# Performance work log

Measured on AMD Instinct MI355X. Metric: run time of the kernel, lower is better.

The kernel has to match this reference:

```python
import jax, jax.numpy as jnp
import numpy as np

B, N, F_IN, F_OUT = 8, 2048, 256, 128
ALPHA = 0.2
NEG_BIG = -9000000000000000.0


def setup_inputs() -> dict:
    key = jax.random.key(0)
    k1, k2, k3, k4 = jax.random.split(key, 4)
    X = jax.random.normal(k1, (B, N, F_IN), dtype=jnp.float32)
    # sparse-ish binary adjacency with self loops (faithful: module only needs 0/1 mask)
    A = (jax.random.uniform(k2, (B, N, N)) < 0.05).astype(jnp.float32)
    eye = jnp.eye(N, dtype=jnp.float32)[None]
    A = jnp.maximum(A, eye)
    # xavier_uniform-style init
    limW = float(np.sqrt(6.0 / (F_IN + F_OUT)))
    W = jax.random.uniform(k3, (F_IN, F_OUT), minval=-limW, maxval=limW, dtype=jnp.float32)
    lima = float(np.sqrt(6.0 / (2 * F_OUT + 1)))
    a = jax.random.uniform(k4, (2 * F_OUT, 1), minval=-lima, maxval=lima, dtype=jnp.float32)
    return {"X": X, "A": A, "W": W, "a": a}


def reference(X, A, W, a):
    # Wh: [B, N, F_OUT]
    Wh = jnp.einsum('bni,io->bno', X, W)
    # split a into source/dest halves: e_ij = leaky_relu(a1.Wh_i + a2.Wh_j)
    # (algebraically identical to cat([Wh_i, Wh_j]) @ a, avoids BxNxNx2F tensor)
    a1 = a[:F_OUT, 0]   # [F_OUT]
    a2 = a[F_OUT:, 0]   # [F_OUT]
    s1 = Wh @ a1        # [B, N]
    s2 = Wh @ a2        # [B, N]
    e = jax.nn.leaky_relu(s1[:, :, None] + s2[:, None, :], negative_slope=ALPHA)  # [B,N,N]
    e = e + NEG_BIG * (1.0 - A)
    attention = jax.nn.softmax(e, axis=-1)
    h_prime = jnp.einsum('bmn,bno->bmo', attention, Wh)
    return h_prime
```

## Files before the change

kernel.cpp:

```cpp
#include <hip/hip_runtime.h>
#include <math.h>

#define B_DIM 8
#define N_DIM 2048
#define F_IN 256
#define F_OUT 128
#define ALPHA 0.2f
#define CAP 256
#define KPAD 136

typedef __attribute__((ext_vector_type(8))) short short8;
typedef __attribute__((ext_vector_type(4))) float floatx4;

static __device__ __forceinline__ unsigned short f2bf(float f) {
    unsigned u = __float_as_uint(f);
    u += 0x7fff + ((u >> 16) & 1);
    return (unsigned short)(u >> 16);
}
static __device__ __forceinline__ float bflo(unsigned w) { return __uint_as_float(w << 16); }
static __device__ __forceinline__ float bfhi(unsigned w) { return __uint_as_float(w & 0xffff0000u); }

__global__ __launch_bounds__(256) void gemm_xw(const float* __restrict__ X,
                                               const float* __restrict__ W,
                                               const float* __restrict__ avec,
                                               unsigned short* __restrict__ Whb,
                                               float* __restrict__ s1,
                                               float* __restrict__ s2) {
    __shared__ unsigned short Wt[F_OUT][KPAD];
    const int t = threadIdx.x;
    const int lane = t & 63, wave = t >> 6;
    const int m = lane & 15, q = lane >> 4;
    const int row0 = blockIdx.x * 64 + wave * 16;

    floatx4 acc[8];
#pragma unroll
    for (int nt = 0; nt < 8; nt++) acc[nt] = (floatx4){0.f, 0.f, 0.f, 0.f};

    const int n0 = (t & 31) * 4;
    const int kb = t >> 5;

    for (int half = 0; half < 2; half++) {
        const float* Wp = W + (size_t)(half * 128 + kb) * F_OUT + n0;
#pragma unroll
        for (int i = 0; i < 16; i++) {
            float4 w = *(const float4*)(Wp + (size_t)i * 8 * F_OUT);
            int kk = kb + i * 8;
            Wt[n0 + 0][kk] = f2bf(w.x);
            Wt[n0 + 1][kk] = f2bf(w.y);
            Wt[n0 + 2][kk] = f2bf(w.z);
            Wt[n0 + 3][kk] = f2bf(w.w);
        }
        __syncthreads();

        const float* xrow = X + (size_t)(row0 + m) * F_IN + half * 128 + q * 8;
        float4 xr[8];
#pragma unroll
        for (int kt = 0; kt < 4; kt++) {
            xr[2 * kt] = *(const float4*)(xrow + kt * 32);
            xr[2 * kt + 1] = *(const float4*)(xrow + kt * 32 + 4);
        }
#pragma unroll
        for (int kt = 0; kt < 4; kt++) {
            union { unsigned short u[8]; short8 v; } af;
            float tmp[8] = {xr[2 * kt].x, xr[2 * kt].y, xr[2 * kt].z, xr[2 * kt].w,
                            xr[2 * kt + 1].x, xr[2 * kt + 1].y, xr[2 * kt + 1].z, xr[2 * kt + 1].w};
#pragma unroll
            for (int j = 0; j < 8; j++) af.u[j] = f2bf(tmp[j]);
#pragma unroll
            for (int nt = 0; nt < 8; nt++) {
                short8 bv = *(const short8*)&Wt[nt * 16 + m][kt * 32 + q * 8];
                acc[nt] = __builtin_amdgcn_mfma_f32_16x16x32_bf16(af.v, bv, acc[nt], 0, 0, 0);
            }
        }
        __syncthreads();
    }

#pragma unroll
    for (int nt = 0; nt < 8; nt++) {
#pragma unroll
        for (int r = 0; r < 4; r++) {
            int row = row0 + q * 4 + r;
            Whb[(size_t)row * F_OUT + nt * 16 + m] = f2bf(acc[nt][r]);
        }
    }
    float a1v[8], a2v[8];
#pragma unroll
    for (int nt = 0; nt < 8; nt++) {
        a1v[nt] = avec[nt * 16 + m];
        a2v[nt] = avec[F_OUT + nt * 16 + m];
    }
#pragma unroll
    for (int r = 0; r < 4; r++) {
        float v1 = 0.f, v2 = 0.f;
#pragma unroll
        for (int nt = 0; nt < 8; nt++) {
            v1 = fmaf(acc[nt][r], a1v[nt], v1);
            v2 = fmaf(acc[nt][r], a2v[nt], v2);
        }
#pragma unroll
        for (int mk = 8; mk >= 1; mk >>= 1) {
            v1 += __shfl_xor(v1, mk, 64);
            v2 += __shfl_xor(v2, mk, 64);
        }
        if (m == 0) {
            int row = row0 + q * 4 + r;
            s1[row] = v1;
            s2[row] = v2;
        }
    }
}

__global__ __launch_bounds__(256) void attn_kernel(const float* __restrict__ A,
                                                   const unsigned short* __restrict__ Whb,
                                                   const float* __restrict__ s1,
                                                   const float* __restrict__ s2,
                                                   float* __restrict__ out) {
    __shared__ __align__(16) float pv[4][CAP * 2];
    __shared__ __align__(16) float s2ls[N_DIM];

    const int t = threadIdx.x;
    const int lane = t & 63, wave = t >> 6;
    const int row = blockIdx.x * 4 + wave;
    const int b = row >> 11;

    {
        const float4* s2g = (const float4*)(s2 + b * N_DIM);
        *(float4*)&s2ls[t * 8] = s2g[t * 2];
        *(float4*)&s2ls[t * 8 + 4] = s2g[t * 2 + 1];
    }
    __syncthreads();

    const float s1m = s1[row];
    const float4* rowA = (const float4*)(A + (size_t)row * N_DIM);

    int base = 0;
    float lmax = -1e30f;
#pragma unroll
    for (int j = 0; j < 8; j++) {
        int idx4 = j * 64 + lane;
        float4 av = rowA[idx4];
        float4 sv = *(const float4*)&s2ls[idx4 * 4];
        float comp[4] = {av.x, av.y, av.z, av.w};
        float svv[4] = {sv.x, sv.y, sv.z, sv.w};
#pragma unroll
        for (int c = 0; c < 4; c++) {
            bool nz = (comp[c] != 0.f);
            unsigned long long mk = __ballot(nz);
            if (nz) {
                float x = s1m + svv[c];
                float e = fmaxf(x, ALPHA * x);
                int r = base + __popcll(mk & ((1ull << lane) - 1ull));
                if (r < CAP) {
                    pv[wave][2 * r] = e;
                    pv[wave][2 * r + 1] = __int_as_float(((idx4 << 2) + c) << 8);
                }
                lmax = fmaxf(lmax, e);
            }
            base += __popcll(mk);
        }
    }
    const int K = base < CAP ? base : CAP;
#pragma unroll
    for (int mk = 32; mk >= 1; mk >>= 1) lmax = fmaxf(lmax, __shfl_xor(lmax, mk, 64));

    float lsum = 0.f;
    for (int k = lane; k < K; k += 64) {
        float p = __expf(pv[wave][2 * k] - lmax);
        pv[wave][2 * k] = p;
        lsum += p;
    }
#pragma unroll
    for (int mk = 32; mk >= 1; mk >>= 1) lsum += __shfl_xor(lsum, mk, 64);
    const float inv = 1.f / lsum;

    const char* Wc = (const char*)(Whb + (size_t)b * N_DIM * F_OUT);
    const int loff = lane * 4;
    float ax = 0.f, ay = 0.f;
    int k = 0;
#pragma unroll 2
    for (; k + 3 < K; k += 4) {
        float4 q0 = *(const float4*)&pv[wave][2 * k];
        float4 q1 = *(const float4*)&pv[wave][2 * k + 4];
        unsigned w0 = *(const unsigned*)(Wc + __float_as_int(q0.y) + loff);
        unsigned w1 = *(const unsigned*)(Wc + __float_as_int(q0.w) + loff);
        unsigned w2 = *(const unsigned*)(Wc + __float_as_int(q1.y) + loff);
        unsigned w3 = *(const unsigned*)(Wc + __float_as_int(q1.w) + loff);
        ax = fmaf(q0.x, bflo(w0), ax); ay = fmaf(q0.x, bfhi(w0), ay);
        ax = fmaf(q0.z, bflo(w1), ax); ay = fmaf(q0.z, bfhi(w1), ay);
        ax = fmaf(q1.x, bflo(w2), ax); ay = fmaf(q1.x, bfhi(w2), ay);
        ax = fmaf(q1.z, bflo(w3), ax); ay = fmaf(q1.z, bfhi(w3), ay);
    }
    for (; k < K; k++) {
        float p = pv[wave][2 * k];
        unsigned w0 = *(const unsigned*)(Wc + __float_as_int(pv[wave][2 * k + 1]) + loff);
        ax = fmaf(p, bflo(w0), ax);
        ay = fmaf(p, bfhi(w0), ay);
    }
    *(float2*)&out[(size_t)row * F_OUT + lane * 2] = make_float2(ax * inv, ay * inv);
}

extern "C" void kernel_launch(void* const* d_in, const int* in_sizes, int n_in,
                              void* d_out, int out_size, void* d_ws, size_t ws_size,
                              hipStream_t stream) {
    const float* X = (const float*)d_in[0];
    const float* A = (const float*)d_in[1];
    const float* W = (const float*)d_in[2];
    const float* avec = (const float*)d_in[3];
    float* out = (float*)d_out;

    unsigned short* Whb = (unsigned short*)d_ws;
    float* s1 = (float*)((char*)d_ws + (size_t)B_DIM * N_DIM * F_OUT * 2);
    float* s2 = s1 + B_DIM * N_DIM;

    gemm_xw<<<B_DIM * N_DIM / 64, 256, 0, stream>>>(X, W, avec, Whb, s1, s2);
    attn_kernel<<<B_DIM * N_DIM / 4, 256, 0, stream>>>(A, Whb, s1, s2, out);
}
```

Measured before the change: 237.4 us.

## Drop shared s2 staging, batch A loads, gather Wh rows with 16-byte loads

The attention kernel no longer stages s2 in shared memory behind a block barrier. It issues all A-row and s2 loads up front into registers so they overlap. The gather-accumulate phase changes from each lane reading 4 bytes per neighbor to 16-lane groups reading 16-byte chunks of four neighbors at once, with a cross-quad shuffle reduction and zero-padded tail entries. This cuts per-neighbor load instruction count and loop overhead, at the cost of more registers and an extra shuffle reduction.

```diff
diff --git a/kernel.cpp b/kernel.cpp
--- a/kernel.cpp
+++ b/kernel.cpp
@@ -115,44 +115,40 @@
                                                    const float* __restrict__ s1,
                                                    const float* __restrict__ s2,
                                                    float* __restrict__ out) {
-    __shared__ __align__(16) float pv[4][CAP * 2];
-    __shared__ __align__(16) float s2ls[N_DIM];
+    __shared__ __align__(16) float pv[4][2 * CAP + 8];
 
     const int t = threadIdx.x;
     const int lane = t & 63, wave = t >> 6;
     const int row = blockIdx.x * 4 + wave;
     const int b = row >> 11;
 
-    {
-        const float4* s2g = (const float4*)(s2 + b * N_DIM);
-        *(float4*)&s2ls[t * 8] = s2g[t * 2];
-        *(float4*)&s2ls[t * 8 + 4] = s2g[t * 2 + 1];
-    }
-    __syncthreads();
-
     const float s1m = s1[row];
     const float4* rowA = (const float4*)(A + (size_t)row * N_DIM);
+    const float4* rowS = (const float4*)(s2 + b * N_DIM);
+
+    float4 av[8], sv[8];
+#pragma unroll
+    for (int j = 0; j < 8; j++) av[j] = rowA[j * 64 + lane];
+#pragma unroll
+    for (int j = 0; j < 8; j++) sv[j] = rowS[j * 64 + lane];
 
     int base = 0;
     float lmax = -1e30f;
 #pragma unroll
     for (int j = 0; j < 8; j++) {
-        int idx4 = j * 64 + lane;
-        float4 av = rowA[idx4];
-        float4 sv = *(const float4*)&s2ls[idx4 * 4];
-        float comp[4] = {av.x, av.y, av.z, av.w};
-        float svv[4] = {sv.x, sv.y, sv.z, sv.w};
+        float ac[4] = {av[j].x, av[j].y, av[j].z, av[j].w};
+        float sc[4] = {sv[j].x, sv[j].y, sv[j].z, sv[j].w};
 #pragma unroll
         for (int c = 0; c < 4; c++) {
-            bool nz = (comp[c] != 0.f);
+            bool nz = (ac[c] != 0.f);
             unsigned long long mk = __ballot(nz);
             if (nz) {
-                float x = s1m + svv[c];
+                float x = s1m + sc[c];
                 float e = fmaxf(x, ALPHA * x);
                 int r = base + __popcll(mk & ((1ull << lane) - 1ull));
                 if (r < CAP) {
-                    pv[wave][2 * r] = e;
-                    pv[wave][2 * r + 1] = __int_as_float(((idx4 << 2) + c) << 8);
+                    *(float2*)&pv[wave][2 * r] =
+                        make_float2(e, __int_as_float((((j * 64 + lane) << 2) + c) << 8));
                 }
                 lmax = fmaxf(lmax, e);
             }
@@ -160,6 +156,7 @@
         }
     }
     const int K = base < CAP ? base : CAP;
+    if (lane < 4) *(float2*)&pv[wave][2 * (K + lane)] = make_float2(0.f, 0.f);
 #pragma unroll
     for (int mk = 32; mk >= 1; mk >>= 1) lmax = fmaxf(lmax, __shfl_xor(lmax, mk, 64));
 
@@ -174,29 +171,37 @@
     const float inv = 1.f / lsum;
 
     const char* Wc = (const char*)(Whb + (size_t)b * N_DIM * F_OUT);
-    const int loff = lane * 4;
-    float ax = 0.f, ay = 0.f;
-    int k = 0;
-#pragma unroll 2
-    for (; k + 3 < K; k += 4) {
-        float4 q0 = *(const float4*)&pv[wave][2 * k];
-        float4 q1 = *(const float4*)&pv[wave][2 * k + 4];
-        unsigned w0 = *(const unsigned*)(Wc + __float_as_int(q0.y) + loff);
-        unsigned w1 = *(const unsigned*)(Wc + __float_as_int(q0.w) + loff);
-        unsigned w2 = *(const unsigned*)(Wc + __float_as_int(q1.y) + loff);
-        unsigned w3 = *(const unsigned*)(Wc + __float_as_int(q1.w) + loff);
-        ax = fmaf(q0.x, bflo(w0), ax); ay = fmaf(q0.x, bfhi(w0), ay);
-        ax = fmaf(q0.z, bflo(w1), ax); ay = fmaf(q0.z, bfhi(w1), ay);
-        ax = fmaf(q1.x, bflo(w2), ax); ay = fmaf(q1.x, bfhi(w2), ay);
-        ax = fmaf(q1.z, bflo(w3), ax); ay = fmaf(q1.z, bfhi(w3), ay);
-    }
-    for (; k < K; k++) {
-        float p = pv[wave][2 * k];
-        unsigned w0 = *(const unsigned*)(Wc + __float_as_int(pv[wave][2 * k + 1]) + loff);
-        ax = fmaf(p, bflo(w0), ax);
-        ay = fmaf(p, bfhi(w0), ay);
-    }
-    *(float2*)&out[(size_t)row * F_OUT + lane * 2] = make_float2(ax * inv, ay * inv);
+    const int qd = lane >> 4, ln = lane & 15;
+    const int loff = ln * 16;
+    float acc[8];
+#pragma unroll
+    for (int j = 0; j < 8; j++) acc[j] = 0.f;
+
+#pragma unroll 4
+    for (int k = 0; k < K; k += 4) {
+        float2 pq = *(const float2*)&pv[wave][2 * (k + qd)];
+        uint4 w = *(const uint4*)(Wc + __float_as_int(pq.y) + loff);
+        const float p = pq.x;
+        acc[0] = fmaf(p, bflo(w.x), acc[0]);
+        acc[1] = fmaf(p, bfhi(w.x), acc[1]);
+        acc[2] = fmaf(p, bflo(w.y), acc[2]);
+        acc[3] = fmaf(p, bfhi(w.y), acc[3]);
+        acc[4] = fmaf(p, bflo(w.z), acc[4]);
+        acc[5] = fmaf(p, bfhi(w.z), acc[5]);
+        acc[6] = fmaf(p, bflo(w.w), acc[6]);
+        acc[7] = fmaf(p, bfhi(w.w), acc[7]);
+    }
+#pragma unroll
+    for (int j = 0; j < 8; j++) {
+        acc[j] += __shfl_xor(acc[j], 32, 64);
+        acc[j] += __shfl_xor(acc[j], 16, 64);
+        acc[j] *= inv;
+    }
+    if (qd == 0) {
+        float* orow = out + (size_t)row * F_OUT + ln * 8;
+        *(float4*)orow = make_float4(acc[0], acc[1], acc[2], acc[3]);
+        *(float4*)(orow + 4) = make_float4(acc[4], acc[5], acc[6], acc[7]);
+    }
 }
 
 extern "C" void kernel_launch(void* const* d_in, const int* in_sizes, int n_in,
```

Result: faster. 229.3 us (-3.4%).

## Replace sparse gather attention with dense MFMA masked-softmax matmul

Applied to the files above, without the earlier changes.

Drops the per-row ballot compaction and gather over nonzero neighbours. The attention output is now a dense bf16 MFMA product of masked exp-probabilities with a transposed Wh. Softmax uses a precomputed upper bound (leaky_relu of s1 plus the per-batch max of s2, collected with atomicMax in the GEMM kernel) instead of a per-row max pass. Partial results from the 8 waves of each block are combined with LDS atomics. The full dense 2048-wide product is computed regardless of sparsity, which adds a memset and risks underflow when the max bound is loose.

```diff
diff --git a/kernel.cpp b/kernel.cpp
--- a/kernel.cpp
+++ b/kernel.cpp
@@ -6,8 +6,8 @@
 #define F_IN 256
 #define F_OUT 128
 #define ALPHA 0.2f
-#define CAP 256
 #define KPAD 136
+#define LSTR 132
 
 typedef __attribute__((ext_vector_type(8))) short short8;
 typedef __attribute__((ext_vector_type(4))) float floatx4;
@@ -17,15 +17,24 @@
     u += 0x7fff + ((u >> 16) & 1);
     return (unsigned short)(u >> 16);
 }
-static __device__ __forceinline__ float bflo(unsigned w) { return __uint_as_float(w << 16); }
-static __device__ __forceinline__ float bfhi(unsigned w) { return __uint_as_float(w & 0xffff0000u); }
+static __device__ __forceinline__ float bf2f(unsigned short s) {
+    return __uint_as_float((unsigned)s << 16);
+}
+static __device__ __forceinline__ unsigned fmap(float f) {
+    int b = __float_as_int(f);
+    return (unsigned)(b ^ ((b >> 31) | 0x80000000));
+}
+static __device__ __forceinline__ float funmap(unsigned u) {
+    return __uint_as_float((u & 0x80000000u) ? (int)(u ^ 0x80000000u) : ~(int)u);
+}
 
 __global__ __launch_bounds__(256) void gemm_xw(const float* __restrict__ X,
                                                const float* __restrict__ W,
                                                const float* __restrict__ avec,
-                                               unsigned short* __restrict__ Whb,
+                                               unsigned short* __restrict__ WhT,
                                                float* __restrict__ s1,
-                                               float* __restrict__ s2) {
+                                               float* __restrict__ s2,
+                                               unsigned* __restrict__ s2max_u) {
     __shared__ unsigned short Wt[F_OUT][KPAD];
     const int t = threadIdx.x;
     const int lane = t & 63, wave = t >> 6;
@@ -75,12 +84,14 @@
         __syncthreads();
     }
 
+    const int b = row0 >> 11;
+    unsigned short* WTb = WhT + (size_t)b * F_OUT * N_DIM;
 #pragma unroll
     for (int nt = 0; nt < 8; nt++) {
 #pragma unroll
         for (int r = 0; r < 4; r++) {
-            int row = row0 + q * 4 + r;
-            Whb[(size_t)row * F_OUT + nt * 16 + m] = f2bf(acc[nt][r]);
+            int nloc = (row0 & 2047) + q * 4 + r;
+            WTb[(size_t)(nt * 16 + m) * N_DIM + nloc] = f2bf(acc[nt][r]);
         }
     }
     float a1v[8], a2v[8];
@@ -89,6 +100,7 @@
         a1v[nt] = avec[nt * 16 + m];
         a2v[nt] = avec[F_OUT + nt * 16 + m];
     }
+    float wmax = -1e30f;
 #pragma unroll
     for (int r = 0; r < 4; r++) {
         float v1 = 0.f, v2 = 0.f;
@@ -107,96 +119,89 @@
             s1[row] = v1;
             s2[row] = v2;
         }
-    }
-}
-
-__global__ __launch_bounds__(256) void attn_kernel(const float* __restrict__ A,
-                                                   const unsigned short* __restrict__ Whb,
-                                                   const float* __restrict__ s1,
-                                                   const float* __restrict__ s2,
-                                                   float* __restrict__ out) {
-    __shared__ __align__(16) float pv[4][CAP * 2];
-    __shared__ __align__(16) float s2ls[N_DIM];
+        wmax = fmaxf(wmax, v2);
+    }
+    wmax = fmaxf(wmax, __shfl_xor(wmax, 16, 64));
+    wmax = fmaxf(wmax, __shfl_xor(wmax, 32, 64));
+    if (lane == 0) atomicMax(&s2max_u[b], fmap(wmax));
+}
+
+__global__ __launch_bounds__(512) void attn_mm(const float* __restrict__ A,
+                                               const unsigned short* __restrict__ WhT,
+                                               const float* __restrict__ s1,
+                                               const float* __restrict__ s2,
+                                               const unsigned* __restrict__ s2max_u,
+                                               float* __restrict__ out) {
+    __shared__ float lred[16 * LSTR + 16];
 
     const int t = threadIdx.x;
     const int lane = t & 63, wave = t >> 6;
-    const int row = blockIdx.x * 4 + wave;
-    const int b = row >> 11;
+    const int m = lane & 15, q = lane >> 4;
+    const int row0 = blockIdx.x * 16;
+    const int b = row0 >> 11;
+    const int nbase = wave * 256;
+
+    for (int i = t; i < 16 * LSTR + 16; i += 512) lred[i] = 0.f;
+
+    const float s1m = s1[row0 + m];
+    const float s2mx = funmap(s2max_u[b]);
+    const float xs = s1m + s2mx;
+    const float shift = fmaxf(xs, ALPHA * xs);
+
+    const float* Ar = A + (size_t)(row0 + m) * N_DIM + nbase + q * 8;
+    const float* s2p = s2 + (size_t)b * N_DIM + nbase + q * 8;
+    const unsigned short* WT = WhT + (size_t)b * F_OUT * N_DIM + nbase + q * 8;
+
+    floatx4 acc[8];
+#pragma unroll
+    for (int nt = 0; nt < 8; nt++) acc[nt] = (floatx4){0.f, 0.f, 0.f, 0.f};
+    float lsum = 0.f;
+
+#pragma unroll
+    for (int s = 0; s < 8; s++) {
+        const int off = s * 32;
+        float4 a0 = *(const float4*)(Ar + off);
+        float4 a1 = *(const float4*)(Ar + off + 4);
+        float4 z0 = *(const float4*)(s2p + off);
+        float4 z1 = *(const float4*)(s2p + off + 4);
+        float aa[8] = {a0.x, a0.y, a0.z, a0.w, a1.x, a1.y, a1.z, a1.w};
+        float zz[8] = {z0.x, z0.y, z0.z, z0.w, z1.x, z1.y, z1.z, z1.w};
+        union { unsigned short u[8]; short8 v; } pf;
+#pragma unroll
+        for (int j = 0; j < 8; j++) {
+            float x = s1m + zz[j];
+            float e = fmaxf(x, ALPHA * x);
+            float p = aa[j] * __expf(e - shift);
+            unsigned short pb = f2bf(p);
+            pf.u[j] = pb;
+            lsum += bf2f(pb);
+        }
+#pragma unroll
+        for (int nt = 0; nt < 8; nt++) {
+            short8 bv = *(const short8*)(WT + (size_t)(nt * 16 + m) * N_DIM + off);
+            acc[nt] = __builtin_amdgcn_mfma_f32_16x16x32_bf16(pf.v, bv, acc[nt], 0, 0, 0);
+        }
+    }
+
+    lsum += __shfl_xor(lsum, 16, 64);
+    lsum += __shfl_xor(lsum, 32, 64);
+
+    __syncthreads();
+    if (lane < 16) atomicAdd(&lred[16 * LSTR + lane], lsum);
+#pragma unroll
+    for (int nt = 0; nt < 8; nt++)
+#pragma unroll
+        for (int r = 0; r < 4; r++)
+            atomicAdd(&lred[(q * 4 + r) * LSTR + nt * 16 + m], acc[nt][r]);
+    __syncthreads();
 
     {
-        const float4* s2g = (const float4*)(s2 + b * N_DIM);
-        *(float4*)&s2ls[t * 8] = s2g[t * 2];
-        *(float4*)&s2ls[t * 8 + 4] = s2g[t * 2 + 1];
-    }
-    __syncthreads();
-
-    const float s1m = s1[row];
-    const float4* rowA = (const float4*)(A + (size_t)row * N_DIM);
-
-    int base = 0;
-    float lmax = -1e30f;
-#pragma unroll
-    for (int j = 0; j < 8; j++) {
-        int idx4 = j * 64 + lane;
-        float4 av = rowA[idx4];
-        float4 sv = *(const float4*)&s2ls[idx4 * 4];
-        float comp[4] = {av.x, av.y, av.z, av.w};
-        float svv[4] = {sv.x, sv.y, sv.z, sv.w};
-#pragma unroll
-        for (int c = 0; c < 4; c++) {
-            bool nz = (comp[c] != 0.f);
-            unsigned long long mk = __ballot(nz);
-            if (nz) {
-                float x = s1m + svv[c];
-                float e = fmaxf(x, ALPHA * x);
-                int r = base + __popcll(mk & ((1ull << lane) - 1ull));
-                if (r < CAP) {
-                    pv[wave][2 * r] = e;
-                    pv[wave][2 * r + 1] = __int_as_float(((idx4 << 2) + c) << 8);
-                }
-                lmax = fmaxf(lmax, e);
-            }
-            base += __popcll(mk);
-        }
-    }
-    const int K = base < CAP ? base : CAP;
-#pragma unroll
-    for (int mk = 32; mk >= 1; mk >>= 1) lmax = fmaxf(lmax, __shfl_xor(lmax, mk, 64));
-
-    float lsum = 0.f;
-    for (int k = lane; k < K; k += 64) {
-        float p = __expf(pv[wave][2 * k] - lmax);
-        pv[wave][2 * k] = p;
-        lsum += p;
-    }
-#pragma unroll
-    for (int mk = 32; mk >= 1; mk >>= 1) lsum += __shfl_xor(lsum, mk, 64);
-    const float inv = 1.f / lsum;
-
-    const char* Wc = (const char*)(Whb + (size_t)b * N_DIM * F_OUT);
-    const int loff = lane * 4;
-    float ax = 0.f, ay = 0.f;
-    int k = 0;
-#pragma unroll 2
-    for (; k + 3 < K; k += 4) {
-        float4 q0 = *(const float4*)&pv[wave][2 * k];
-        float4 q1 = *(const float4*)&pv[wave][2 * k + 4];
-        unsigned w0 = *(const unsigned*)(Wc + __float_as_int(q0.y) + loff);
-        unsigned w1 = *(const unsigned*)(Wc + __float_as_int(q0.w) + loff);
-        unsigned w2 = *(const unsigned*)(Wc + __float_as_int(q1.y) + loff);
-        unsigned w3 = *(const unsigned*)(Wc + __float_as_int(q1.w) + loff);
-        ax = fmaf(q0.x, bflo(w0), ax); ay = fmaf(q0.x, bfhi(w0), ay);
-        ax = fmaf(q0.z, bflo(w1), ax); ay = fmaf(q0.z, bfhi(w1), ay);
-        ax = fmaf(q1.x, bflo(w2), ax); ay = fmaf(q1.x, bfhi(w2), ay);
-        ax = fmaf(q1.z, bflo(w3), ax); ay = fmaf(q1.z, bfhi(w3), ay);
-    }
-    for (; k < K; k++) {
-        float p = pv[wave][2 * k];
-        unsigned w0 = *(const unsigned*)(Wc + __float_as_int(pv[wave][2 * k + 1]) + loff);
-        ax = fmaf(p, bflo(w0), ax);
-        ay = fmaf(p, bfhi(w0), ay);
-    }
-    *(float2*)&out[(size_t)row * F_OUT + lane * 2] = make_float2(ax * inv, ay * inv);
+        int r = t >> 5, c0 = (t & 31) * 4;
+        float inv = 1.f / lred[16 * LSTR + r];
+        float4 v = *(const float4*)&lred[r * LSTR + c0];
+        v.x *= inv; v.y *= inv; v.z *= inv; v.w *= inv;
+        *(float4*)&out[(size_t)(row0 + r) * F_OUT + c0] = v;
+    }
 }
 
 extern "C" void kernel_launch(void* const* d_in, const int* in_sizes, int n_in,
@@ -208,10 +213,12 @@
     const float* avec = (const float*)d_in[3];
     float* out = (float*)d_out;
 
-    unsigned short* Whb = (unsigned short*)d_ws;
-    float* s1 = (float*)((char*)d_ws + (size_t)B_DIM * N_DIM * F_OUT * 2);
+    unsigned short* WhT = (unsigned short*)d_ws;
+    float* s1 = (float*)((char*)d_ws + (size_t)B_DIM * F_OUT * N_DIM * 2);
     float* s2 = s1 + B_DIM * N_DIM;
-
-    gemm_xw<<<B_DIM * N_DIM / 64, 256, 0, stream>>>(X, W, avec, Whb, s1, s2);
-    attn_kernel<<<B_DIM * N_DIM / 4, 256, 0, stream>>>(A, Whb, s1, s2, out);
-}
+    unsigned* s2max_u = (unsigned*)(s2 + B_DIM * N_DIM);
+
+    hipMemsetAsync(s2max_u, 0, B_DIM * sizeof(unsigned), stream);
+    gemm_xw<<<B_DIM * N_DIM / 64, 256, 0, stream>>>(X, W, avec, WhT, s1, s2, s2max_u);
+    attn_mm<<<B_DIM * N_DIM / 16, 512, 0, stream>>>(A, WhT, s1, s2, s2max_u, out);
+}
```

Result: slower. 363.0 us (+52.9%).
